# Performance work log

Hardware: AMD Instinct MI355X
Metric: run time of the kernel (lower is better)

## Reference

```python
import jax, jax.numpy as jnp
import numpy as np

MV = 16  # multivector dimension of the Clifford algebra (Cl(1,3))

def setup_inputs() -> dict:
    key = jax.random.key(0)
    k1, k2, k3 = jax.random.split(key, 3)
    gp = jax.random.normal(k1, (MV, MV, MV), dtype=jnp.float32)  # Cayley table [i,j,k]
    x = jax.random.normal(k2, (2048, 256, MV), dtype=jnp.float32)  # [a,b,j]
    y = jax.random.normal(k3, (2048, 256, MV), dtype=jnp.float32)  # [a,b,k]
    return {"gp": gp, "x": x, "y": y}

def reference(gp, x, y):
    # Original: out1 = einsum('ijk,abj->abik', gp, x); out = einsum('abik,abk->abi', out1, y)
    # Fused into a single contraction (identical math, avoids the [a,b,i,k] intermediate):
    return jnp.einsum('ijk,abj,abk->abi', gp, x, y)
```

## Files before the change

### kernel.cpp

```cpp
#include <hip/hip_runtime.h>

#define MV 16

typedef __attribute__((ext_vector_type(8))) short short8;
typedef __attribute__((ext_vector_type(4))) float f32x4;

template <int TPW, bool GUARD>
__global__ __launch_bounds__(256) void gp_fused_kernel(
    const float* __restrict__ gp,
    const float* __restrict__ x,
    const float* __restrict__ y,
    float* __restrict__ out,
    int ntiles)
{
    __shared__ unsigned short ldsb[4096];

    const int tid  = threadIdx.x;
    const int lane = tid & 63;
    const int wid  = tid >> 6;
    const int g    = lane >> 4;
    const int p    = lane & 15;
    const int ja   = g >> 1;
    const int kb   = g & 1;

    const float4* gsrc = reinterpret_cast<const float4*>(gp) + tid * 4;
    float4 g0 = gsrc[0], g1 = gsrc[1], g2 = gsrc[2], g3 = gsrc[3];

    const int tile0 = (blockIdx.x * 4 + wid) * TPW;
    const size_t xoff = (size_t)p * MV + 8 * ja;
    const size_t yoff = (size_t)p * MV + 8 * kb;

    float4 xa[TPW][2], ya[TPW][2];
    #pragma unroll
    for (int t = 0; t < TPW; ++t) {
        if (!GUARD || tile0 + t < ntiles) {
            const float* xp = x + (size_t)(tile0 + t) * 16 * MV + xoff;
            const float* yp = y + (size_t)(tile0 + t) * 16 * MV + yoff;
            xa[t][0] = *reinterpret_cast<const float4*>(xp);
            xa[t][1] = *reinterpret_cast<const float4*>(xp + 4);
            ya[t][0] = *reinterpret_cast<const float4*>(yp);
            ya[t][1] = *reinterpret_cast<const float4*>(yp + 4);
        }
    }

    {
        float gf[16] = {g0.x, g0.y, g0.z, g0.w, g1.x, g1.y, g1.z, g1.w,
                        g2.x, g2.y, g2.z, g2.w, g3.x, g3.y, g3.z, g3.w};
        short8 lo, hi;
        #pragma unroll
        for (int e = 0; e < 8; ++e) {
            __bf16 hl = (__bf16)gf[e];
            __bf16 hh = (__bf16)gf[e + 8];
            lo[e] = __builtin_bit_cast(short, hl);
            hi[e] = __builtin_bit_cast(short, hh);
        }
        const int i = tid >> 4, j = tid & 15;
        const int c = j & 7, jaw = j >> 3;
        unsigned short* d0 = ldsb + ((c * 64 + 32 * jaw) + i) * 8;
        *reinterpret_cast<short8*>(d0)       = lo;
        *reinterpret_cast<short8*>(d0 + 128) = hi;
    }
    __syncthreads();

    short8 bfrag[8];
    #pragma unroll
    for (int c = 0; c < 8; ++c)
        bfrag[c] = *reinterpret_cast<const short8*>(ldsb + (c * 64 + lane) * 8);

    #pragma unroll
    for (int t = 0; t < TPW; ++t) {
        if (GUARD && tile0 + t >= ntiles) continue;

        float xs[8] = {xa[t][0].x, xa[t][0].y, xa[t][0].z, xa[t][0].w,
                       xa[t][1].x, xa[t][1].y, xa[t][1].z, xa[t][1].w};
        float ys[8] = {ya[t][0].x, ya[t][0].y, ya[t][0].z, ya[t][0].w,
                       ya[t][1].x, ya[t][1].y, ya[t][1].z, ya[t][1].w};

        f32x4 acc = {0.f, 0.f, 0.f, 0.f};
        #pragma unroll
        for (int c = 0; c < 8; ++c) {
            float xj = xs[c];
            short8 a;
            #pragma unroll
            for (int e = 0; e < 8; ++e) {
                __bf16 h = (__bf16)(xj * ys[e]);
                a[e] = __builtin_bit_cast(short, h);
            }
            acc = __builtin_amdgcn_mfma_f32_16x16x32_bf16(a, bfrag[c], acc, 0, 0, 0);
        }

        float* op = out + ((size_t)(tile0 + t) * 16 + 4 * g) * MV + p;
        op[0 * MV] = acc[0];
        op[1 * MV] = acc[1];
        op[2 * MV] = acc[2];
        op[3 * MV] = acc[3];
    }
}

__global__ __launch_bounds__(256) void gp_fp32_kernel(
    const float* __restrict__ g,
    const float* __restrict__ x,
    const float* __restrict__ y,
    float* __restrict__ out,
    int npix)
{
    int idx = blockIdx.x * blockDim.x + threadIdx.x;
    if (idx >= npix) return;

    const float4* xv = reinterpret_cast<const float4*>(x) + (size_t)idx * 4;
    const float4* yv = reinterpret_cast<const float4*>(y) + (size_t)idx * 4;

    float xr[MV], yr[MV], acc[MV];
    #pragma unroll
    for (int q = 0; q < 4; ++q) {
        float4 t = xv[q];
        xr[4*q+0] = t.x; xr[4*q+1] = t.y; xr[4*q+2] = t.z; xr[4*q+3] = t.w;
        float4 u = yv[q];
        yr[4*q+0] = u.x; yr[4*q+1] = u.y; yr[4*q+2] = u.z; yr[4*q+3] = u.w;
    }
    #pragma unroll
    for (int i = 0; i < MV; ++i) acc[i] = 0.0f;

    #pragma unroll
    for (int j = 0; j < MV; ++j) {
        #pragma unroll
        for (int k = 0; k < MV; ++k) {
            float pr = xr[j] * yr[k];
            #pragma unroll
            for (int i = 0; i < MV; ++i)
                acc[i] = fmaf(g[(i * MV + j) * MV + k], pr, acc[i]);
        }
    }

    float4* ov = reinterpret_cast<float4*>(out) + (size_t)idx * 4;
    #pragma unroll
    for (int q = 0; q < 4; ++q)
        ov[q] = make_float4(acc[4*q+0], acc[4*q+1], acc[4*q+2], acc[4*q+3]);
}

extern "C" void kernel_launch(void* const* d_in, const int* in_sizes, int n_in,
                              void* d_out, int out_size, void* d_ws, size_t ws_size,
                              hipStream_t stream) {
    const float* gp = (const float*)d_in[0];
    const float* x  = (const float*)d_in[1];
    const float* y  = (const float*)d_in[2];
    float* out      = (float*)d_out;

    int npix = in_sizes[1] / MV;
    constexpr int TPW = 4;

    if ((npix % 16) == 0) {
        int ntiles = npix / 16;
        if (ntiles % (4 * TPW) == 0) {
            int blocks = ntiles / (4 * TPW);
            gp_fused_kernel<TPW, false><<<blocks, 256, 0, stream>>>(gp, x, y, out, ntiles);
        } else {
            int blocks = (ntiles + 4 * TPW - 1) / (4 * TPW);
            gp_fused_kernel<TPW, true><<<blocks, 256, 0, stream>>>(gp, x, y, out, ntiles);
        }
    } else {
        int blocks = (npix + 255) / 256;
        gp_fp32_kernel<<<blocks, 256, 0, stream>>>(gp, x, y, out, npix);
    }
}
```

Measured before the change: 22.32 us.

## Add double-buffered pipelined kernel processing eight tiles per wave

Adds a new kernel in which each wave handles eight tiles, and the x/y loads for the next pair of tiles are issued while the current pair is computed with MFMA. The goal is to overlap global memory latency with compute and to spread the per-block setup cost (the Cayley table load, bf16 conversion and LDS staging) over more tiles. In exchange there are half as many blocks, which may leave fewer waves available to hide latency across the GPU, and register use rises from holding the double buffer. The existing fallback kernel is reduced to an always-guarded version.

```diff
diff --git a/kernel.cpp b/kernel.cpp
--- a/kernel.cpp
+++ b/kernel.cpp
@@ -5,7 +5,111 @@
 typedef __attribute__((ext_vector_type(8))) short short8;
 typedef __attribute__((ext_vector_type(4))) float f32x4;
 
-template <int TPW, bool GUARD>
+template <int TPWAVE>
+__global__ __launch_bounds__(256, 4) void gp_pipe_kernel(
+    const float* __restrict__ gp,
+    const float* __restrict__ x,
+    const float* __restrict__ y,
+    float* __restrict__ out)
+{
+    __shared__ unsigned short ldsb[4096];
+
+    const int tid  = threadIdx.x;
+    const int lane = tid & 63;
+    const int wid  = tid >> 6;
+    const int g    = lane >> 4;
+    const int p    = lane & 15;
+    const int ja   = g >> 1;
+    const int kb   = g & 1;
+
+    const float4* gsrc = reinterpret_cast<const float4*>(gp) + tid * 4;
+    float4 g0 = gsrc[0], g1 = gsrc[1], g2 = gsrc[2], g3 = gsrc[3];
+
+    const int   tile0 = (blockIdx.x * 4 + wid) * TPWAVE;
+    const size_t xoff = (size_t)p * MV + 8 * ja;
+    const size_t yoff = (size_t)p * MV + 8 * kb;
+
+    float4 fx0[2][2], fx1[2][2], fy0[2][2], fy1[2][2];
+
+#define LOADTILE(B, T, TILE)                                                   \
+    do {                                                                       \
+        const float* xp_ = x + (size_t)(TILE) * 16 * MV + xoff;                \
+        const float* yp_ = y + (size_t)(TILE) * 16 * MV + yoff;                \
+        fx0[B][T] = *reinterpret_cast<const float4*>(xp_);                     \
+        fx1[B][T] = *reinterpret_cast<const float4*>(xp_ + 4);                 \
+        fy0[B][T] = *reinterpret_cast<const float4*>(yp_);                     \
+        fy1[B][T] = *reinterpret_cast<const float4*>(yp_ + 4);                 \
+    } while (0)
+
+    LOADTILE(0, 0, tile0 + 0);
+    LOADTILE(0, 1, tile0 + 1);
+
+    {
+        float gf[16] = {g0.x, g0.y, g0.z, g0.w, g1.x, g1.y, g1.z, g1.w,
+                        g2.x, g2.y, g2.z, g2.w, g3.x, g3.y, g3.z, g3.w};
+        short8 lo, hi;
+        #pragma unroll
+        for (int e = 0; e < 8; ++e) {
+            __bf16 hl = (__bf16)gf[e];
+            __bf16 hh = (__bf16)gf[e + 8];
+            lo[e] = __builtin_bit_cast(short, hl);
+            hi[e] = __builtin_bit_cast(short, hh);
+        }
+        const int i = tid >> 4, j = tid & 15;
+        const int c = j & 7, jaw = j >> 3;
+        unsigned short* d0 = ldsb + ((c * 64 + 32 * jaw) + i) * 8;
+        *reinterpret_cast<short8*>(d0)       = lo;
+        *reinterpret_cast<short8*>(d0 + 128) = hi;
+    }
+    __syncthreads();
+
+    short8 bfrag[8];
+    #pragma unroll
+    for (int c = 0; c < 8; ++c)
+        bfrag[c] = *reinterpret_cast<const short8*>(ldsb + (c * 64 + lane) * 8);
+
+    constexpr int P = TPWAVE / 2;
+    #pragma unroll
+    for (int s = 0; s < P; ++s) {
+        const int cur = s & 1, nxt = cur ^ 1;
+
+        if (s + 1 < P) {
+            LOADTILE(nxt, 0, tile0 + 2 * (s + 1) + 0);
+            LOADTILE(nxt, 1, tile0 + 2 * (s + 1) + 1);
+        }
+
+        #pragma unroll
+        for (int tt = 0; tt < 2; ++tt) {
+            const int tile = tile0 + 2 * s + tt;
+            float xs[8] = {fx0[cur][tt].x, fx0[cur][tt].y, fx0[cur][tt].z, fx0[cur][tt].w,
+                           fx1[cur][tt].x, fx1[cur][tt].y, fx1[cur][tt].z, fx1[cur][tt].w};
+            float ys[8] = {fy0[cur][tt].x, fy0[cur][tt].y, fy0[cur][tt].z, fy0[cur][tt].w,
+                           fy1[cur][tt].x, fy1[cur][tt].y, fy1[cur][tt].z, fy1[cur][tt].w};
+
+            f32x4 acc = {0.f, 0.f, 0.f, 0.f};
+            #pragma unroll
+            for (int c = 0; c < 8; ++c) {
+                float xj = xs[c];
+                short8 a;
+                #pragma unroll
+                for (int e = 0; e < 8; ++e) {
+                    __bf16 h = (__bf16)(xj * ys[e]);
+                    a[e] = __builtin_bit_cast(short, h);
+                }
+                acc = __builtin_amdgcn_mfma_f32_16x16x32_bf16(a, bfrag[c], acc, 0, 0, 0);
+            }
+
+            float* op = out + ((size_t)tile * 16 + 4 * g) * MV + p;
+            op[0 * MV] = acc[0];
+            op[1 * MV] = acc[1];
+            op[2 * MV] = acc[2];
+            op[3 * MV] = acc[3];
+        }
+    }
+#undef LOADTILE
+}
+
+template <int TPW>
 __global__ __launch_bounds__(256) void gp_fused_kernel(
     const float* __restrict__ gp,
     const float* __restrict__ x,
@@ -33,7 +137,7 @@
     float4 xa[TPW][2], ya[TPW][2];
     #pragma unroll
     for (int t = 0; t < TPW; ++t) {
-        if (!GUARD || tile0 + t < ntiles) {
+        if (tile0 + t < ntiles) {
             const float* xp = x + (size_t)(tile0 + t) * 16 * MV + xoff;
             const float* yp = y + (size_t)(tile0 + t) * 16 * MV + yoff;
             xa[t][0] = *reinterpret_cast<const float4*>(xp);
@@ -69,7 +173,7 @@
 
     #pragma unroll
     for (int t = 0; t < TPW; ++t) {
-        if (GUARD && tile0 + t >= ntiles) continue;
+        if (tile0 + t >= ntiles) continue;
 
         float xs[8] = {xa[t][0].x, xa[t][0].y, xa[t][0].z, xa[t][0].w,
                        xa[t][1].x, xa[t][1].y, xa[t][1].z, xa[t][1].w};
@@ -147,16 +251,17 @@
     float* out      = (float*)d_out;
 
     int npix = in_sizes[1] / MV;
-    constexpr int TPW = 4;
+    constexpr int TPWAVE = 8;
 
     if ((npix % 16) == 0) {
         int ntiles = npix / 16;
-        if (ntiles % (4 * TPW) == 0) {
-            int blocks = ntiles / (4 * TPW);
-            gp_fused_kernel<TPW, false><<<blocks, 256, 0, stream>>>(gp, x, y, out, ntiles);
+        if (ntiles % (4 * TPWAVE) == 0) {
+            int blocks = ntiles / (4 * TPWAVE);
+            gp_pipe_kernel<TPWAVE><<<blocks, 256, 0, stream>>>(gp, x, y, out);
         } else {
+            constexpr int TPW = 4;
             int blocks = (ntiles + 4 * TPW - 1) / (4 * TPW);
-            gp_fused_kernel<TPW, true><<<blocks, 256, 0, stream>>>(gp, x, y, out, ntiles);
+            gp_fused_kernel<TPW><<<blocks, 256, 0, stream>>>(gp, x, y, out, ntiles);
         }
     } else {
         int blocks = (npix + 255) / 256;
```

Measured after the change: 21.17 us. 5.2% less time.
